# Performance work log

Hardware: AMD Instinct MI355X
Metric: run time of the kernel (lower is better)

## Reference

```python
import jax, jax.numpy as jnp
import numpy as np

B, C, W, H = 16, 256, 32, 32  # L = W*H = 1024
NUM_HEAD = 4
DIM_HEAD = C  # dim_head defaults to in_channels


def setup_inputs() -> dict:
    key = jax.random.key(0)
    ks = jax.random.split(key, 6)
    s = 0.02  # small init scale, like trained linear weights
    return {
        "x": jax.random.normal(ks[0], (B, C, W, H), dtype=jnp.float32),
        "Wq": jax.random.normal(ks[1], (NUM_HEAD, DIM_HEAD, C), dtype=jnp.float32) * s,
        "Wk": jax.random.normal(ks[2], (NUM_HEAD, DIM_HEAD, C), dtype=jnp.float32) * s,
        "Wv": jax.random.normal(ks[3], (NUM_HEAD, DIM_HEAD, C), dtype=jnp.float32) * s,
        "Wo_w": jax.random.normal(ks[4], (C, NUM_HEAD * DIM_HEAD), dtype=jnp.float32) * s,
        "Wo_b": jax.random.normal(ks[5], (C,), dtype=jnp.float32) * s,
    }


def reference(x, Wq, Wk, Wv, Wo_w, Wo_b):
    b, c, w, h = x.shape
    L = w * h
    # [b,c,w,h] -> [b,L,c]
    xs = jnp.transpose(x, (0, 2, 3, 1)).reshape(b, L, c)
    # per-head projections (torch Linear: y = x @ W^T), batched over heads
    Q = jnp.einsum('blc,hdc->bhld', xs, Wq)
    K = jnp.einsum('blc,hdc->bhld', xs, Wk)
    V = jnp.einsum('blc,hdc->bhld', xs, Wv)
    # no softmax: scores = Q K^T, heads = scores V
    scores = jnp.einsum('bhld,bhmd->bhlm', Q, K)  # [b,H,L,L]
    heads = jnp.einsum('bhlm,bhmd->bhld', scores, V)  # [b,H,L,d]
    # concat heads along channel dim -> [b,L,H*d], then output projection
    cat = jnp.transpose(heads, (0, 2, 1, 3)).reshape(b, L, -1)
    z = cat @ Wo_w.T + Wo_b  # [b,L,c]
    return jnp.transpose(z, (0, 2, 1)).reshape(b, c, w, h)
```

## Files before the change

### kernel.cpp

```cpp
#include <hip/hip_runtime.h>
#include <hip/hip_bf16.h>

typedef __attribute__((ext_vector_type(8))) short s8v;
typedef __attribute__((ext_vector_type(4))) float f4v;

__device__ __forceinline__ ushort f2bf(float f) {
    __hip_bfloat16 h = __float2bfloat16(f);
    return __builtin_bit_cast(ushort, h);
}

__device__ __forceinline__ int fsw(int row) { return ((row >> 1) ^ (row >> 3)) & 3; }

__device__ __forceinline__ void gload16(const ushort* g, ushort* l) {
    __builtin_amdgcn_global_load_lds(
        (const __attribute__((address_space(1))) unsigned*)g,
        (__attribute__((address_space(3))) unsigned*)l, 16, 0, 0);
}

__device__ __forceinline__ void cvtw16(ushort* p, float4 a, float4 b) {
    s8v u;
    u[0] = (short)f2bf(a.x); u[1] = (short)f2bf(a.y);
    u[2] = (short)f2bf(a.z); u[3] = (short)f2bf(a.w);
    u[4] = (short)f2bf(b.x); u[5] = (short)f2bf(b.y);
    u[6] = (short)f2bf(b.z); u[7] = (short)f2bf(b.w);
    *(s8v*)p = u;
}

__device__ __forceinline__ void scatw(ushort* L, int c8, int d, float4 a, float4 b) {
    float v[8] = { a.x, a.y, a.z, a.w, b.x, b.y, b.z, b.w };
#pragma unroll
    for (int i = 0; i < 8; ++i) {
        int row = c8 + i;
        L[row * 32 + (((d >> 3) ^ fsw(row)) << 3) + (d & 7)] = f2bf(v[i]);
    }
}

__device__ __forceinline__ void gemmS(
    const float* __restrict__ Xb, ushort* lds, int row0, int col0,
    ushort* __restrict__ S, int mirror) {
    const int NT = 16;
    const int tid = threadIdx.x, wave = tid >> 6, lane = tid & 63;
    const int g = wave >> 2, w4 = wave & 3;
    const int wr = w4 >> 1, wc = w4 & 1;
    const int rA = lane & 15, kg = lane >> 4;
    const int tg = tid & 255;
    const int srow = tg >> 2, slot = tg & 3;
    const int kb = g * (NT * 32);
    ushort* LA = lds + g * 16384;
    ushort* LB = LA + 8192;
    const int wadr = srow * 32 + ((slot ^ fsw(srow)) << 3);
    const float* gx = Xb + (size_t)(row0 + srow) * 1024 + kb + slot * 8;
    const float* gy = Xb + (size_t)(col0 + srow) * 1024 + kb + slot * 8;
    f4v acc[2][2] = {};
    __syncthreads();

    float4 bx[4][2], by[4][2];
#pragma unroll
    for (int p = 0; p < 3; ++p) {
        bx[p][0] = *(const float4*)(gx + p * 32);
        bx[p][1] = *(const float4*)(gx + p * 32 + 4);
        by[p][0] = *(const float4*)(gy + p * 32);
        by[p][1] = *(const float4*)(gy + p * 32 + 4);
    }
    cvtw16(LA + wadr, bx[0][0], bx[0][1]);
    cvtw16(LB + wadr, by[0][0], by[0][1]);

#pragma unroll
    for (int t = 0; t < NT; ++t) {
        if (t + 3 < NT) {
            const int bi = (t + 3) & 3;
            bx[bi][0] = *(const float4*)(gx + (t + 3) * 32);
            bx[bi][1] = *(const float4*)(gx + (t + 3) * 32 + 4);
            by[bi][0] = *(const float4*)(gy + (t + 3) * 32);
            by[bi][1] = *(const float4*)(gy + (t + 3) * 32 + 4);
        }
        if (t + 1 < NT) {
            const int bi = (t + 1) & 3;
            cvtw16(LA + ((t + 1) & 3) * 2048 + wadr, bx[bi][0], bx[bi][1]);
            cvtw16(LB + ((t + 1) & 3) * 2048 + wadr, by[bi][0], by[bi][1]);
        }
        asm volatile("s_waitcnt lgkmcnt(0)" ::: "memory");
        __builtin_amdgcn_s_barrier();
        __builtin_amdgcn_sched_barrier(0);
        const ushort* pa = LA + (t & 3) * 2048;
        const ushort* pb = LB + (t & 3) * 2048;
        s8v a[2], b[2];
#pragma unroll
        for (int m = 0; m < 2; ++m) {
            int row = wr * 32 + m * 16 + rA;
            a[m] = *(const s8v*)&pa[row * 32 + ((kg ^ fsw(row)) << 3)];
        }
#pragma unroll
        for (int n = 0; n < 2; ++n) {
            int row = wc * 32 + n * 16 + rA;
            b[n] = *(const s8v*)&pb[row * 32 + ((kg ^ fsw(row)) << 3)];
        }
#pragma unroll
        for (int m = 0; m < 2; ++m)
#pragma unroll
            for (int n = 0; n < 2; ++n)
                acc[m][n] = __builtin_amdgcn_mfma_f32_16x16x32_bf16(a[m], b[n], acc[m][n], 0, 0, 0);
    }
    __syncthreads();
    float* red = (float*)lds;
    if (g == 1) {
#pragma unroll
        for (int m = 0; m < 2; ++m)
#pragma unroll
            for (int n = 0; n < 2; ++n)
                *(f4v*)&red[(w4 * 64 + lane) * 16 + (m * 2 + n) * 4] = acc[m][n];
    }
    __syncthreads();
    if (g == 0) {
        int r4 = (lane >> 4) * 4, cl = lane & 15;
#pragma unroll
        for (int m = 0; m < 2; ++m)
#pragma unroll
            for (int n = 0; n < 2; ++n) {
                f4v o = *(const f4v*)&red[(w4 * 64 + lane) * 16 + (m * 2 + n) * 4];
                f4v s = acc[m][n] + o;
                int row = row0 + wr * 32 + m * 16 + r4;
                int col = col0 + wc * 32 + n * 16 + cl;
                ushort4 tv = { f2bf(s[0]), f2bf(s[1]), f2bf(s[2]), f2bf(s[3]) };
                S[(size_t)(row + 0) * 256 + col] = tv.x;
                S[(size_t)(row + 1) * 256 + col] = tv.y;
                S[(size_t)(row + 2) * 256 + col] = tv.z;
                S[(size_t)(row + 3) * 256 + col] = tv.w;
                if (mirror)
                    *(ushort4*)&S[(size_t)col * 256 + row] = tv;
            }
    }
}

template<int XT>
__device__ __forceinline__ void gemmWT(
    const float* __restrict__ Xw, const float* __restrict__ Yw,
    ushort* lds, int row0, int col0, ushort* __restrict__ O, int ldo) {
    const int NT = 4;
    const int tid = threadIdx.x, wave = tid >> 6, lane = tid & 63;
    const int g = wave >> 2, w4 = wave & 3;
    const int wr = w4 >> 1, wc = w4 & 1;
    const int rA = lane & 15, kg = lane >> 4;
    const int tg = tid & 255;
    const int kb = g * 128;
    ushort* LA = lds + g * 16384;
    ushort* LB = LA + 8192;
    const int dT = tg >> 3, c8 = (tg & 7) * 8;
    const int srow = tg >> 2, slot = tg & 3;
    const int wadr = srow * 32 + ((slot ^ fsw(srow)) << 3);
    f4v acc[2][2] = {};
    __syncthreads();

    float4 bx[4][2], by[4][2];
#pragma unroll
    for (int p = 0; p < 3; ++p) {
        if (XT) {
            bx[p][0] = *(const float4*)(Xw + (size_t)(kb + p * 32 + dT) * 256 + row0 + c8);
            bx[p][1] = *(const float4*)(Xw + (size_t)(kb + p * 32 + dT) * 256 + row0 + c8 + 4);
        } else {
            bx[p][0] = *(const float4*)(Xw + (size_t)(row0 + srow) * 1024 + kb + p * 32 + slot * 8);
            bx[p][1] = *(const float4*)(Xw + (size_t)(row0 + srow) * 1024 + kb + p * 32 + slot * 8 + 4);
        }
        by[p][0] = *(const float4*)(Yw + (size_t)(kb + p * 32 + dT) * 256 + col0 + c8);
        by[p][1] = *(const float4*)(Yw + (size_t)(kb + p * 32 + dT) * 256 + col0 + c8 + 4);
    }
    if (XT) scatw(LA, c8, dT, bx[0][0], bx[0][1]);
    else    cvtw16(LA + wadr, bx[0][0], bx[0][1]);
    scatw(LB, c8, dT, by[0][0], by[0][1]);

#pragma unroll
    for (int t = 0; t < NT; ++t) {
        if (t + 3 < NT) {
            const int bi = (t + 3) & 3;
            if (XT) {
                bx[bi][0] = *(const float4*)(Xw + (size_t)(kb + (t + 3) * 32 + dT) * 256 + row0 + c8);
                bx[bi][1] = *(const float4*)(Xw + (size_t)(kb + (t + 3) * 32 + dT) * 256 + row0 + c8 + 4);
            } else {
                bx[bi][0] = *(const float4*)(Xw + (size_t)(row0 + srow) * 1024 + kb + (t + 3) * 32 + slot * 8);
                bx[bi][1] = *(const float4*)(Xw + (size_t)(row0 + srow) * 1024 + kb + (t + 3) * 32 + slot * 8 + 4);
            }
            by[bi][0] = *(const float4*)(Yw + (size_t)(kb + (t + 3) * 32 + dT) * 256 + col0 + c8);
            by[bi][1] = *(const float4*)(Yw + (size_t)(kb + (t + 3) * 32 + dT) * 256 + col0 + c8 + 4);
        }
        if (t + 1 < NT) {
            const int bi = (t + 1) & 3;
            ushort* la = LA + ((t + 1) & 3) * 2048;
            ushort* lb = LB + ((t + 1) & 3) * 2048;
            if (XT) scatw(la, c8, dT, bx[bi][0], bx[bi][1]);
            else    cvtw16(la + wadr, bx[bi][0], bx[bi][1]);
            scatw(lb, c8, dT, by[bi][0], by[bi][1]);
        }
        asm volatile("s_waitcnt lgkmcnt(0)" ::: "memory");
        __builtin_amdgcn_s_barrier();
        __builtin_amdgcn_sched_barrier(0);
        const ushort* pa = LA + (t & 3) * 2048;
        const ushort* pb = LB + (t & 3) * 2048;
        s8v a[2], b[2];
#pragma unroll
        for (int m = 0; m < 2; ++m) {
            int row = wr * 32 + m * 16 + rA;
            a[m] = *(const s8v*)&pa[row * 32 + ((kg ^ fsw(row)) << 3)];
        }
#pragma unroll
        for (int n = 0; n < 2; ++n) {
            int row = wc * 32 + n * 16 + rA;
            b[n] = *(const s8v*)&pb[row * 32 + ((kg ^ fsw(row)) << 3)];
        }
#pragma unroll
        for (int m = 0; m < 2; ++m)
#pragma unroll
            for (int n = 0; n < 2; ++n)
                acc[m][n] = __builtin_amdgcn_mfma_f32_16x16x32_bf16(a[m], b[n], acc[m][n], 0, 0, 0);
    }
    __syncthreads();
    float* red = (float*)lds;
    if (g == 1) {
#pragma unroll
        for (int m = 0; m < 2; ++m)
#pragma unroll
            for (int n = 0; n < 2; ++n)
                *(f4v*)&red[(w4 * 64 + lane) * 16 + (m * 2 + n) * 4] = acc[m][n];
    }
    __syncthreads();
    if (g == 0) {
        int r4 = (lane >> 4) * 4, cl = lane & 15;
#pragma unroll
        for (int m = 0; m < 2; ++m)
#pragma unroll
            for (int n = 0; n < 2; ++n) {
                f4v o = *(const f4v*)&red[(w4 * 64 + lane) * 16 + (m * 2 + n) * 4];
                f4v s = acc[m][n] + o;
                int row = row0 + wr * 32 + m * 16 + r4;
                int col = col0 + wc * 32 + n * 16 + cl;
#pragma unroll
                for (int r = 0; r < 4; ++r)
                    O[(size_t)(row + r) * ldo + col] = f2bf(s[r]);
            }
    }
}

__device__ __forceinline__ void gemm64x8(
    const ushort* __restrict__ Xb, const ushort* __restrict__ Yb,
    int ldx, int ldy, ushort* lds, int row0, int col0, int K,
    ushort* __restrict__ O, int ldo) {
    const int tid = threadIdx.x, wave = tid >> 6, lane = tid & 63;
    const int g = wave >> 2, w4 = wave & 3;
    const int wr = w4 >> 1, wc = w4 & 1;
    const int rA = lane & 15, kg = lane >> 4;
    const int srow = w4 * 16 + (lane >> 2);
    const int scol = ((lane & 3) ^ fsw(srow)) * 8;
    const int K2 = K >> 1, NT = K2 >> 5, kb = g * K2;
    ushort* LA = lds + g * 16384;
    ushort* LB = LA + 8192;
    f4v acc[2][2] = {};
    __syncthreads();
    const ushort* gx = Xb + (size_t)(row0 + srow) * ldx + kb + scol;
    const ushort* gy = Yb + (size_t)(col0 + srow) * ldy + kb + scol;
    gload16(gx,      LA + w4 * 512);
    gload16(gy,      LB + w4 * 512);
    gload16(gx + 32, LA + 2048 + w4 * 512);
    gload16(gy + 32, LB + 2048 + w4 * 512);
    for (int t = 0; t < NT; ++t) {
        if (t + 2 < NT) {
            int s2 = (t + 2) & 3, kt = (t + 2) << 5;
            gload16(gx + kt, LA + s2 * 2048 + w4 * 512);
            gload16(gy + kt, LB + s2 * 2048 + w4 * 512);
            asm volatile("s_waitcnt vmcnt(4)" ::: "memory");
        } else if (t + 1 < NT) {
            asm volatile("s_waitcnt vmcnt(2)" ::: "memory");
        } else {
            asm volatile("s_waitcnt vmcnt(0)" ::: "memory");
        }
        __builtin_amdgcn_s_barrier();
        __builtin_amdgcn_sched_barrier(0);
        const ushort* pa = LA + (t & 3) * 2048;
        const ushort* pb = LB + (t & 3) * 2048;
        s8v a[2], b[2];
#pragma unroll
        for (int m = 0; m < 2; ++m) {
            int row = wr * 32 + m * 16 + rA;
            a[m] = *(const s8v*)&pa[row * 32 + ((kg ^ fsw(row)) << 3)];
        }
#pragma unroll
        for (int n = 0; n < 2; ++n) {
            int row = wc * 32 + n * 16 + rA;
            b[n] = *(const s8v*)&pb[row * 32 + ((kg ^ fsw(row)) << 3)];
        }
#pragma unroll
        for (int m = 0; m < 2; ++m)
#pragma unroll
            for (int n = 0; n < 2; ++n)
                acc[m][n] = __builtin_amdgcn_mfma_f32_16x16x32_bf16(a[m], b[n], acc[m][n], 0, 0, 0);
    }
    __syncthreads();
    float* red = (float*)lds;
    if (g == 1) {
#pragma unroll
        for (int m = 0; m < 2; ++m)
#pragma unroll
            for (int n = 0; n < 2; ++n)
                *(f4v*)&red[(w4 * 64 + lane) * 16 + (m * 2 + n) * 4] = acc[m][n];
    }
    __syncthreads();
    if (g == 0) {
        int r4 = (lane >> 4) * 4, cl = lane & 15;
#pragma unroll
        for (int m = 0; m < 2; ++m)
#pragma unroll
            for (int n = 0; n < 2; ++n) {
                f4v o = *(const f4v*)&red[(w4 * 64 + lane) * 16 + (m * 2 + n) * 4];
                f4v s = acc[m][n] + o;
                int row = row0 + wr * 32 + m * 16 + r4;
                int col = col0 + wc * 32 + n * 16 + cl;
#pragma unroll
                for (int r = 0; r < 4; ++r)
                    O[(size_t)(row + r) * ldo + col] = f2bf(s[r]);
            }
    }
}

template<int OBF>
__device__ __forceinline__ void gemm128x8(
    const ushort* __restrict__ Xb, const ushort* __restrict__ Yb,
    int ldx, int ldy, ushort* lds, int row0, int col0, int K,
    void* __restrict__ Oraw, int ldo, const float* __restrict__ bias) {
    const int tid = threadIdx.x, wave = tid >> 6, lane = tid & 63;
    const int wr = wave >> 2, wc = wave & 3;
    const int rA = lane & 15, kg = lane >> 4;
    const int srow = wave * 16 + (lane >> 2);
    const int scol = ((lane & 3) ^ fsw(srow)) * 8;
    const int NT = K >> 5;
    ushort* LA = lds;
    ushort* LB = lds + 16384;
    f4v acc[4][2] = {};
    __syncthreads();
    const ushort* gx = Xb + (size_t)(row0 + srow) * ldx + scol;
    const ushort* gy = Yb + (size_t)(col0 + srow) * ldy + scol;
#pragma unroll
    for (int p = 0; p < 2; ++p) {
        gload16(gx + p * 32, LA + p * 4096 + wave * 512);
        gload16(gy + p * 32, LB + p * 4096 + wave * 512);
    }
    for (int t = 0; t < NT; ++t) {
        if (t + 2 < NT) {
            int s2 = (t + 2) & 3, kt = (t + 2) << 5;
            gload16(gx + kt, LA + s2 * 4096 + wave * 512);
            gload16(gy + kt, LB + s2 * 4096 + wave * 512);
            asm volatile("s_waitcnt vmcnt(4)" ::: "memory");
        } else if (t + 1 < NT) {
            asm volatile("s_waitcnt vmcnt(2)" ::: "memory");
        } else {
            asm volatile("s_waitcnt vmcnt(0)" ::: "memory");
        }
        __builtin_amdgcn_s_barrier();
        __builtin_amdgcn_sched_barrier(0);
        const ushort* pa = LA + (t & 3) * 4096;
        const ushort* pb = LB + (t & 3) * 4096;
        s8v a[4], b[2];
#pragma unroll
        for (int m = 0; m < 4; ++m) {
            int row = wr * 64 + m * 16 + rA;
            a[m] = *(const s8v*)&pa[row * 32 + ((kg ^ fsw(row)) << 3)];
        }
#pragma unroll
        for (int n = 0; n < 2; ++n) {
            int row = wc * 32 + n * 16 + rA;
            b[n] = *(const s8v*)&pb[row * 32 + ((kg ^ fsw(row)) << 3)];
        }
#pragma unroll
        for (int m = 0; m < 4; ++m)
#pragma unroll
            for (int n = 0; n < 2; ++n)
                acc[m][n] = __builtin_amdgcn_mfma_f32_16x16x32_bf16(a[m], b[n], acc[m][n], 0, 0, 0);
    }
    int r4 = (lane >> 4) * 4, cl = lane & 15;
    if (OBF) {
        ushort* O = (ushort*)Oraw;
#pragma unroll
        for (int m = 0; m < 4; ++m)
#pragma unroll
            for (int n = 0; n < 2; ++n) {
                int row = row0 + wr * 64 + m * 16 + r4;
                int col = col0 + wc * 32 + n * 16 + cl;
#pragma unroll
                for (int r = 0; r < 4; ++r)
                    O[(size_t)(row + r) * ldo + col] = f2bf(acc[m][n][r]);
            }
    } else {
        float* O = (float*)Oraw;
#pragma unroll
        for (int m = 0; m < 4; ++m)
#pragma unroll
            for (int n = 0; n < 2; ++n) {
                int row = row0 + wr * 64 + m * 16 + r4;
                int col = col0 + wc * 32 + n * 16 + cl;
#pragma unroll
                for (int r = 0; r < 4; ++r)
                    O[(size_t)(row + r) * ldo + col] = acc[m][n][r] + bias[row + r];
            }
    }
}

__global__ __launch_bounds__(512, 2) void kSP(
    const float* __restrict__ x, const float* __restrict__ Wq,
    const float* __restrict__ Wk,
    ushort* __restrict__ S16, ushort* __restrict__ A16, ushort* __restrict__ xlc) {
    __shared__ __align__(16) ushort lds[32768];
    const int bid = blockIdx.x, tid = threadIdx.x;
    if (bid < 160) {
        int xcd = bid & 7, idx = bid >> 3;
        int b = 2 * xcd + (idx >= 10);
        int tri = (idx >= 10) ? idx - 10 : idx;
        int ti, tj;
        if (tri < 4)      { ti = 0; tj = tri; }
        else if (tri < 7) { ti = 1; tj = tri - 3; }
        else if (tri < 9) { ti = 2; tj = tri - 5; }
        else              { ti = 3; tj = 3; }
        const float* xb = x + (size_t)b * 262144;
        gemmS(xb, lds, ti * 64, tj * 64, S16 + (size_t)b * 65536, ti != tj);
    } else if (bid < 224) {
        int q = bid - 160, h = q >> 4, t2 = q & 15;
        gemmWT<1>(Wq + (size_t)h * 65536, Wk + (size_t)h * 65536, lds,
                  (t2 >> 2) * 64, (t2 & 3) * 64, A16 + (size_t)h * 65536, 256);
    } else {
        ushort (*t)[72] = (ushort(*)[72])lds;
        int r = tid >> 3, c0 = (tid & 7) * 8;
#pragma unroll
        for (int rr = 0; rr < 4; ++rr) {
            int jid = (bid - 224) + 256 * rr;
            __syncthreads();
            int lt = jid & 15, ct = (jid >> 4) & 3, b2 = jid >> 6;
            size_t so = (size_t)(b2 * 256 + ct * 64 + r) * 1024 + lt * 64 + c0;
            float4 v0 = *(const float4*)(x + so);
            float4 v1 = *(const float4*)(x + so + 4);
            ushort4 u0 = { f2bf(v0.x), f2bf(v0.y), f2bf(v0.z), f2bf(v0.w) };
            ushort4 u1 = { f2bf(v1.x), f2bf(v1.y), f2bf(v1.z), f2bf(v1.w) };
            *(ushort4*)&t[r][c0] = u0;
            *(ushort4*)&t[r][c0 + 4] = u1;
            __syncthreads();
            size_t dof = (size_t)(b2 * 1024 + lt * 64 + r) * 256 + ct * 64 + c0;
            ushort4 w0 = { t[c0][r], t[c0 + 1][r], t[c0 + 2][r], t[c0 + 3][r] };
            ushort4 w1 = { t[c0 + 4][r], t[c0 + 5][r], t[c0 + 6][r], t[c0 + 7][r] };
            *(ushort4*)(xlc + dof) = w0;
            *(ushort4*)(xlc + dof + 4) = w1;
        }
    }
}

__global__ __launch_bounds__(512, 2) void kT1(
    const ushort* __restrict__ A16, const ushort* __restrict__ S16,
    const float* __restrict__ Wo, const float* __restrict__ Wv,
    ushort* __restrict__ T1, ushort* __restrict__ BT) {
    __shared__ __align__(16) ushort lds[32768];
    int j = blockIdx.x;
    if (j < 256) {
        int xcd = j & 7, idx = j >> 3;
        int b = 2 * xcd + (idx >> 4), h = (idx >> 2) & 3, tile = idx & 3;
        gemm128x8<1>(A16 + (size_t)h * 65536, S16 + (size_t)b * 65536, 256, 256, lds,
                     (tile >> 1) * 128, (tile & 1) * 128, 256,
                     T1 + (size_t)b * 262144 + h * 256, 1024, nullptr);
    } else {
        int q = j - 256, h = q >> 4, t2 = q & 15;
        gemmWT<0>(Wo + (size_t)h * 256, Wv + (size_t)h * 65536, lds,
                  (t2 >> 2) * 64, (t2 & 3) * 64, BT + (size_t)h * 256, 1024);
    }
}

__global__ __launch_bounds__(512, 2) void kGT(
    const ushort* __restrict__ BT, const ushort* __restrict__ T1,
    ushort* __restrict__ GT) {
    __shared__ __align__(16) ushort lds[32768];
    int j = blockIdx.x, xcd = j & 7, idx = j >> 3;
    int b = 2 * xcd + (idx >> 4), tile = idx & 15;
    gemm64x8(BT, T1 + (size_t)b * 262144, 1024, 1024, lds,
             (tile >> 2) * 64, (tile & 3) * 64, 1024, GT + (size_t)b * 65536, 256);
}

__global__ __launch_bounds__(512, 2) void kOUT(
    const ushort* __restrict__ GT, const ushort* __restrict__ xlc,
    float* __restrict__ out, const float* __restrict__ bias) {
    __shared__ __align__(16) ushort lds[32768];
    int j = blockIdx.x, xcd = j & 7, idx = j >> 3;
    int b = 2 * xcd + (idx >> 4), tile = idx & 15;
    gemm128x8<0>(GT + (size_t)b * 65536, xlc + (size_t)b * 262144, 256, 256, lds,
                 (tile >> 3) * 128, (tile & 7) * 128, 256,
                 out + (size_t)b * 262144, 1024, bias);
}

extern "C" void kernel_launch(void* const* d_in, const int* in_sizes, int n_in,
                              void* d_out, int out_size, void* d_ws, size_t ws_size,
                              hipStream_t stream) {
    const float* x  = (const float*)d_in[0];
    const float* Wq = (const float*)d_in[1];
    const float* Wk = (const float*)d_in[2];
    const float* Wv = (const float*)d_in[3];
    const float* Wo = (const float*)d_in[4];
    const float* Wb = (const float*)d_in[5];

    char* ws = (char*)d_ws;
    ushort* T1  = (ushort*)(ws + 0);
    ushort* xlc = (ushort*)(ws + 8388608);
    ushort* S16 = (ushort*)(ws + 16777216);
    ushort* GT  = (ushort*)(ws + 20971520);
    ushort* A16 = (ushort*)(ws + 25165824);
    ushort* BT  = (ushort*)(ws + 26214400);

    hipLaunchKernelGGL(kSP,  dim3(480), dim3(512), 0, stream, x, Wq, Wk, S16, A16, xlc);
    hipLaunchKernelGGL(kT1,  dim3(320), dim3(512), 0, stream, A16, S16, Wo, Wv, T1, BT);
    hipLaunchKernelGGL(kGT,  dim3(256), dim3(512), 0, stream, BT, T1, GT);
    hipLaunchKernelGGL(kOUT, dim3(256), dim3(512), 0, stream, GT, xlc, (float*)d_out, Wb);
}
```

Baseline: 39.82 us.

## Replace LDS-staged GEMMs with direct-to-register per-wave MFMA tiles; move BT build into kSP

Three bf16 GEMM kernels (kT1, kGT, kOUT) stop staging tiles through LDS with global_load_lds, barriers and a split-K reduction. Each wave now computes its own 64x64 or 32x32 output tile, loading MFMA operand fragments straight from global memory into a register ring buffer a few k-steps ahead. Blocks shrink to 256 threads. The Wo·Wv (BT) GEMM moves from kT1 into the first kernel kSP, so it runs alongside the other weight preprocessing. The trade is no LDS operand reuse across waves, more global/L2 traffic with uncoalesced 16-byte row loads, and more register pressure.

```diff
diff --git a/kernel.cpp b/kernel.cpp
--- a/kernel.cpp
+++ b/kernel.cpp
@@ -10,12 +10,6 @@
 }
 
 __device__ __forceinline__ int fsw(int row) { return ((row >> 1) ^ (row >> 3)) & 3; }
-
-__device__ __forceinline__ void gload16(const ushort* g, ushort* l) {
-    __builtin_amdgcn_global_load_lds(
-        (const __attribute__((address_space(1))) unsigned*)g,
-        (__attribute__((address_space(3))) unsigned*)l, 16, 0, 0);
-}
 
 __device__ __forceinline__ void cvtw16(ushort* p, float4 a, float4 b) {
     s8v u;
@@ -34,6 +28,8 @@
         L[row * 32 + (((d >> 3) ^ fsw(row)) << 3) + (d & 7)] = f2bf(v[i]);
     }
 }
+
+__device__ __forceinline__ s8v ld8(const ushort* p) { return *(const s8v*)p; }
 
 __device__ __forceinline__ void gemmS(
     const float* __restrict__ Xb, ushort* lds, int row0, int col0,
@@ -239,149 +235,49 @@
     }
 }
 
-__device__ __forceinline__ void gemm64x8(
-    const ushort* __restrict__ Xb, const ushort* __restrict__ Yb,
-    int ldx, int ldy, ushort* lds, int row0, int col0, int K,
-    ushort* __restrict__ O, int ldo) {
-    const int tid = threadIdx.x, wave = tid >> 6, lane = tid & 63;
-    const int g = wave >> 2, w4 = wave & 3;
-    const int wr = w4 >> 1, wc = w4 & 1;
+template<int NT, int OBF>
+__device__ __forceinline__ void gemmDF64(
+    const ushort* __restrict__ X, const ushort* __restrict__ Y,
+    int ldx, int ldy, int row0, int col0,
+    void* __restrict__ Oraw, int ldo, const float* __restrict__ bias) {
+    const int lane = threadIdx.x & 63;
     const int rA = lane & 15, kg = lane >> 4;
-    const int srow = w4 * 16 + (lane >> 2);
-    const int scol = ((lane & 3) ^ fsw(srow)) * 8;
-    const int K2 = K >> 1, NT = K2 >> 5, kb = g * K2;
-    ushort* LA = lds + g * 16384;
-    ushort* LB = LA + 8192;
-    f4v acc[2][2] = {};
-    __syncthreads();
-    const ushort* gx = Xb + (size_t)(row0 + srow) * ldx + kb + scol;
-    const ushort* gy = Yb + (size_t)(col0 + srow) * ldy + kb + scol;
-    gload16(gx,      LA + w4 * 512);
-    gload16(gy,      LB + w4 * 512);
-    gload16(gx + 32, LA + 2048 + w4 * 512);
-    gload16(gy + 32, LB + 2048 + w4 * 512);
+    const ushort* ax = X + (size_t)(row0 + rA) * ldx + kg * 8;
+    const ushort* by = Y + (size_t)(col0 + rA) * ldy + kg * 8;
+    f4v acc[4][4] = {};
+    s8v a[3][4], b[3][4];
+#pragma unroll
+    for (int p = 0; p < 2; ++p) {
+#pragma unroll
+        for (int m = 0; m < 4; ++m) a[p][m] = ld8(ax + (size_t)m * 16 * ldx + p * 32);
+#pragma unroll
+        for (int n = 0; n < 4; ++n) b[p][n] = ld8(by + (size_t)n * 16 * ldy + p * 32);
+    }
+#pragma unroll
     for (int t = 0; t < NT; ++t) {
         if (t + 2 < NT) {
-            int s2 = (t + 2) & 3, kt = (t + 2) << 5;
-            gload16(gx + kt, LA + s2 * 2048 + w4 * 512);
-            gload16(gy + kt, LB + s2 * 2048 + w4 * 512);
-            asm volatile("s_waitcnt vmcnt(4)" ::: "memory");
-        } else if (t + 1 < NT) {
-            asm volatile("s_waitcnt vmcnt(2)" ::: "memory");
-        } else {
-            asm volatile("s_waitcnt vmcnt(0)" ::: "memory");
-        }
-        __builtin_amdgcn_s_barrier();
-        __builtin_amdgcn_sched_barrier(0);
-        const ushort* pa = LA + (t & 3) * 2048;
-        const ushort* pb = LB + (t & 3) * 2048;
-        s8v a[2], b[2];
-#pragma unroll
-        for (int m = 0; m < 2; ++m) {
-            int row = wr * 32 + m * 16 + rA;
-            a[m] = *(const s8v*)&pa[row * 32 + ((kg ^ fsw(row)) << 3)];
-        }
-#pragma unroll
-        for (int n = 0; n < 2; ++n) {
-            int row = wc * 32 + n * 16 + rA;
-            b[n] = *(const s8v*)&pb[row * 32 + ((kg ^ fsw(row)) << 3)];
-        }
-#pragma unroll
-        for (int m = 0; m < 2; ++m)
-#pragma unroll
-            for (int n = 0; n < 2; ++n)
-                acc[m][n] = __builtin_amdgcn_mfma_f32_16x16x32_bf16(a[m], b[n], acc[m][n], 0, 0, 0);
-    }
-    __syncthreads();
-    float* red = (float*)lds;
-    if (g == 1) {
-#pragma unroll
-        for (int m = 0; m < 2; ++m)
-#pragma unroll
-            for (int n = 0; n < 2; ++n)
-                *(f4v*)&red[(w4 * 64 + lane) * 16 + (m * 2 + n) * 4] = acc[m][n];
-    }
-    __syncthreads();
-    if (g == 0) {
-        int r4 = (lane >> 4) * 4, cl = lane & 15;
-#pragma unroll
-        for (int m = 0; m < 2; ++m)
-#pragma unroll
-            for (int n = 0; n < 2; ++n) {
-                f4v o = *(const f4v*)&red[(w4 * 64 + lane) * 16 + (m * 2 + n) * 4];
-                f4v s = acc[m][n] + o;
-                int row = row0 + wr * 32 + m * 16 + r4;
-                int col = col0 + wc * 32 + n * 16 + cl;
-#pragma unroll
-                for (int r = 0; r < 4; ++r)
-                    O[(size_t)(row + r) * ldo + col] = f2bf(s[r]);
-            }
-    }
-}
-
-template<int OBF>
-__device__ __forceinline__ void gemm128x8(
-    const ushort* __restrict__ Xb, const ushort* __restrict__ Yb,
-    int ldx, int ldy, ushort* lds, int row0, int col0, int K,
-    void* __restrict__ Oraw, int ldo, const float* __restrict__ bias) {
-    const int tid = threadIdx.x, wave = tid >> 6, lane = tid & 63;
-    const int wr = wave >> 2, wc = wave & 3;
-    const int rA = lane & 15, kg = lane >> 4;
-    const int srow = wave * 16 + (lane >> 2);
-    const int scol = ((lane & 3) ^ fsw(srow)) * 8;
-    const int NT = K >> 5;
-    ushort* LA = lds;
-    ushort* LB = lds + 16384;
-    f4v acc[4][2] = {};
-    __syncthreads();
-    const ushort* gx = Xb + (size_t)(row0 + srow) * ldx + scol;
-    const ushort* gy = Yb + (size_t)(col0 + srow) * ldy + scol;
-#pragma unroll
-    for (int p = 0; p < 2; ++p) {
-        gload16(gx + p * 32, LA + p * 4096 + wave * 512);
-        gload16(gy + p * 32, LB + p * 4096 + wave * 512);
-    }
-    for (int t = 0; t < NT; ++t) {
-        if (t + 2 < NT) {
-            int s2 = (t + 2) & 3, kt = (t + 2) << 5;
-            gload16(gx + kt, LA + s2 * 4096 + wave * 512);
-            gload16(gy + kt, LB + s2 * 4096 + wave * 512);
-            asm volatile("s_waitcnt vmcnt(4)" ::: "memory");
-        } else if (t + 1 < NT) {
-            asm volatile("s_waitcnt vmcnt(2)" ::: "memory");
-        } else {
-            asm volatile("s_waitcnt vmcnt(0)" ::: "memory");
-        }
-        __builtin_amdgcn_s_barrier();
-        __builtin_amdgcn_sched_barrier(0);
-        const ushort* pa = LA + (t & 3) * 4096;
-        const ushort* pb = LB + (t & 3) * 4096;
-        s8v a[4], b[2];
-#pragma unroll
-        for (int m = 0; m < 4; ++m) {
-            int row = wr * 64 + m * 16 + rA;
-            a[m] = *(const s8v*)&pa[row * 32 + ((kg ^ fsw(row)) << 3)];
-        }
-#pragma unroll
-        for (int n = 0; n < 2; ++n) {
-            int row = wc * 32 + n * 16 + rA;
-            b[n] = *(const s8v*)&pb[row * 32 + ((kg ^ fsw(row)) << 3)];
-        }
+            const int s = (t + 2) % 3;
+#pragma unroll
+            for (int m = 0; m < 4; ++m) a[s][m] = ld8(ax + (size_t)m * 16 * ldx + (t + 2) * 32);
+#pragma unroll
+            for (int n = 0; n < 4; ++n) b[s][n] = ld8(by + (size_t)n * 16 * ldy + (t + 2) * 32);
+        }
+        const int c = t % 3;
 #pragma unroll
         for (int m = 0; m < 4; ++m)
 #pragma unroll
-            for (int n = 0; n < 2; ++n)
-                acc[m][n] = __builtin_amdgcn_mfma_f32_16x16x32_bf16(a[m], b[n], acc[m][n], 0, 0, 0);
-    }
-    int r4 = (lane >> 4) * 4, cl = lane & 15;
+            for (int n = 0; n < 4; ++n)
+                acc[m][n] = __builtin_amdgcn_mfma_f32_16x16x32_bf16(a[c][m], b[c][n], acc[m][n], 0, 0, 0);
+    }
+    const int r4 = (lane >> 4) * 4, cl = lane & 15;
     if (OBF) {
         ushort* O = (ushort*)Oraw;
 #pragma unroll
         for (int m = 0; m < 4; ++m)
 #pragma unroll
-            for (int n = 0; n < 2; ++n) {
-                int row = row0 + wr * 64 + m * 16 + r4;
-                int col = col0 + wc * 32 + n * 16 + cl;
+            for (int n = 0; n < 4; ++n) {
+                int row = row0 + m * 16 + r4;
+                int col = col0 + n * 16 + cl;
 #pragma unroll
                 for (int r = 0; r < 4; ++r)
                     O[(size_t)(row + r) * ldo + col] = f2bf(acc[m][n][r]);
@@ -391,9 +287,9 @@
 #pragma unroll
         for (int m = 0; m < 4; ++m)
 #pragma unroll
-            for (int n = 0; n < 2; ++n) {
-                int row = row0 + wr * 64 + m * 16 + r4;
-                int col = col0 + wc * 32 + n * 16 + cl;
+            for (int n = 0; n < 4; ++n) {
+                int row = row0 + m * 16 + r4;
+                int col = col0 + n * 16 + cl;
 #pragma unroll
                 for (int r = 0; r < 4; ++r)
                     O[(size_t)(row + r) * ldo + col] = acc[m][n][r] + bias[row + r];
@@ -401,10 +297,58 @@
     }
 }
 
+template<int NT>
+__device__ __forceinline__ void gemmDF32(
+    const ushort* __restrict__ X, const ushort* __restrict__ Y,
+    int ldx, int ldy, int row0, int col0, ushort* __restrict__ O, int ldo) {
+    const int lane = threadIdx.x & 63;
+    const int rA = lane & 15, kg = lane >> 4;
+    const ushort* ax = X + (size_t)(row0 + rA) * ldx + kg * 8;
+    const ushort* by = Y + (size_t)(col0 + rA) * ldy + kg * 8;
+    f4v acc[2][2] = {};
+    s8v a[4][2], b[4][2];
+#pragma unroll
+    for (int p = 0; p < 3; ++p) {
+#pragma unroll
+        for (int m = 0; m < 2; ++m) a[p][m] = ld8(ax + (size_t)m * 16 * ldx + p * 32);
+#pragma unroll
+        for (int n = 0; n < 2; ++n) b[p][n] = ld8(by + (size_t)n * 16 * ldy + p * 32);
+    }
+#pragma unroll
+    for (int t = 0; t < NT; ++t) {
+        if (t + 3 < NT) {
+            const int s = (t + 3) & 3;
+#pragma unroll
+            for (int m = 0; m < 2; ++m) a[s][m] = ld8(ax + (size_t)m * 16 * ldx + (t + 3) * 32);
+#pragma unroll
+            for (int n = 0; n < 2; ++n) b[s][n] = ld8(by + (size_t)n * 16 * ldy + (t + 3) * 32);
+        }
+        const int c = t & 3;
+#pragma unroll
+        for (int m = 0; m < 2; ++m)
+#pragma unroll
+            for (int n = 0; n < 2; ++n)
+                acc[m][n] = __builtin_amdgcn_mfma_f32_16x16x32_bf16(a[c][m], b[c][n], acc[m][n], 0, 0, 0);
+    }
+    const int r4 = (lane >> 4) * 4, cl = lane & 15;
+#pragma unroll
+    for (int m = 0; m < 2; ++m)
+#pragma unroll
+        for (int n = 0; n < 2; ++n) {
+            int row = row0 + m * 16 + r4;
+            int col = col0 + n * 16 + cl;
+#pragma unroll
+            for (int r = 0; r < 4; ++r)
+                O[(size_t)(row + r) * ldo + col] = f2bf(acc[m][n][r]);
+        }
+}
+
 __global__ __launch_bounds__(512, 2) void kSP(
     const float* __restrict__ x, const float* __restrict__ Wq,
-    const float* __restrict__ Wk,
-    ushort* __restrict__ S16, ushort* __restrict__ A16, ushort* __restrict__ xlc) {
+    const float* __restrict__ Wk, const float* __restrict__ Wv,
+    const float* __restrict__ Wo,
+    ushort* __restrict__ S16, ushort* __restrict__ A16,
+    ushort* __restrict__ BT, ushort* __restrict__ xlc) {
     __shared__ __align__(16) ushort lds[32768];
     const int bid = blockIdx.x, tid = threadIdx.x;
     if (bid < 160) {
@@ -422,12 +366,16 @@
         int q = bid - 160, h = q >> 4, t2 = q & 15;
         gemmWT<1>(Wq + (size_t)h * 65536, Wk + (size_t)h * 65536, lds,
                   (t2 >> 2) * 64, (t2 & 3) * 64, A16 + (size_t)h * 65536, 256);
+    } else if (bid < 288) {
+        int q = bid - 224, h = q >> 4, t2 = q & 15;
+        gemmWT<0>(Wo + (size_t)h * 256, Wv + (size_t)h * 65536, lds,
+                  (t2 >> 2) * 64, (t2 & 3) * 64, BT + (size_t)h * 256, 1024);
     } else {
         ushort (*t)[72] = (ushort(*)[72])lds;
         int r = tid >> 3, c0 = (tid & 7) * 8;
 #pragma unroll
         for (int rr = 0; rr < 4; ++rr) {
-            int jid = (bid - 224) + 256 * rr;
+            int jid = (bid - 288) + 256 * rr;
             __syncthreads();
             int lt = jid & 15, ct = (jid >> 4) & 3, b2 = jid >> 6;
             size_t so = (size_t)(b2 * 256 + ct * 64 + r) * 1024 + lt * 64 + c0;
@@ -447,44 +395,40 @@
     }
 }
 
-__global__ __launch_bounds__(512, 2) void kT1(
+__global__ __launch_bounds__(256, 2) void kT1(
     const ushort* __restrict__ A16, const ushort* __restrict__ S16,
-    const float* __restrict__ Wo, const float* __restrict__ Wv,
-    ushort* __restrict__ T1, ushort* __restrict__ BT) {
-    __shared__ __align__(16) ushort lds[32768];
-    int j = blockIdx.x;
-    if (j < 256) {
-        int xcd = j & 7, idx = j >> 3;
-        int b = 2 * xcd + (idx >> 4), h = (idx >> 2) & 3, tile = idx & 3;
-        gemm128x8<1>(A16 + (size_t)h * 65536, S16 + (size_t)b * 65536, 256, 256, lds,
-                     (tile >> 1) * 128, (tile & 1) * 128, 256,
-                     T1 + (size_t)b * 262144 + h * 256, 1024, nullptr);
-    } else {
-        int q = j - 256, h = q >> 4, t2 = q & 15;
-        gemmWT<0>(Wo + (size_t)h * 256, Wv + (size_t)h * 65536, lds,
-                  (t2 >> 2) * 64, (t2 & 3) * 64, BT + (size_t)h * 256, 1024);
-    }
-}
-
-__global__ __launch_bounds__(512, 2) void kGT(
+    ushort* __restrict__ T1) {
+    int bid = blockIdx.x, wave = threadIdx.x >> 6;
+    int xcd = bid & 7, idx = bid >> 3;
+    int b = 2 * xcd + (idx >> 4);
+    int tile = (idx & 15) * 4 + wave;
+    int h = tile >> 4, r = (tile >> 2) & 3, c = tile & 3;
+    gemmDF64<8, 1>(A16 + (size_t)h * 65536, S16 + (size_t)b * 65536, 256, 256,
+                   r * 64, c * 64, T1 + (size_t)b * 262144 + h * 256, 1024, nullptr);
+}
+
+__global__ __launch_bounds__(256, 2) void kGT(
     const ushort* __restrict__ BT, const ushort* __restrict__ T1,
     ushort* __restrict__ GT) {
-    __shared__ __align__(16) ushort lds[32768];
-    int j = blockIdx.x, xcd = j & 7, idx = j >> 3;
-    int b = 2 * xcd + (idx >> 4), tile = idx & 15;
-    gemm64x8(BT, T1 + (size_t)b * 262144, 1024, 1024, lds,
-             (tile >> 2) * 64, (tile & 3) * 64, 1024, GT + (size_t)b * 65536, 256);
-}
-
-__global__ __launch_bounds__(512, 2) void kOUT(
+    int bid = blockIdx.x, wave = threadIdx.x >> 6;
+    int xcd = bid & 7, idx = bid >> 3;
+    int b = 2 * xcd + (idx >> 4);
+    int tile = (idx & 15) * 4 + wave;
+    int rt = tile >> 3, ct = tile & 7;
+    gemmDF32<32>(BT, T1 + (size_t)b * 262144, 1024, 1024,
+                 rt * 32, ct * 32, GT + (size_t)b * 65536, 256);
+}
+
+__global__ __launch_bounds__(256, 2) void kOUT(
     const ushort* __restrict__ GT, const ushort* __restrict__ xlc,
     float* __restrict__ out, const float* __restrict__ bias) {
-    __shared__ __align__(16) ushort lds[32768];
-    int j = blockIdx.x, xcd = j & 7, idx = j >> 3;
-    int b = 2 * xcd + (idx >> 4), tile = idx & 15;
-    gemm128x8<0>(GT + (size_t)b * 65536, xlc + (size_t)b * 262144, 256, 256, lds,
-                 (tile >> 3) * 128, (tile & 7) * 128, 256,
-                 out + (size_t)b * 262144, 1024, bias);
+    int bid = blockIdx.x, wave = threadIdx.x >> 6;
+    int xcd = bid & 7, idx = bid >> 3;
+    int b = 2 * xcd + (idx >> 4);
+    int tile = (idx & 15) * 4 + wave;
+    int rt = tile >> 4, ct = tile & 15;
+    gemmDF64<8, 0>(GT + (size_t)b * 65536, xlc + (size_t)b * 262144, 256, 256,
+                   rt * 64, ct * 64, out + (size_t)b * 262144, 1024, bias);
 }
 
 extern "C" void kernel_launch(void* const* d_in, const int* in_sizes, int n_in,
@@ -505,8 +449,9 @@
     ushort* A16 = (ushort*)(ws + 25165824);
     ushort* BT  = (ushort*)(ws + 26214400);
 
-    hipLaunchKernelGGL(kSP,  dim3(480), dim3(512), 0, stream, x, Wq, Wk, S16, A16, xlc);
-    hipLaunchKernelGGL(kT1,  dim3(320), dim3(512), 0, stream, A16, S16, Wo, Wv, T1, BT);
-    hipLaunchKernelGGL(kGT,  dim3(256), dim3(512), 0, stream, BT, T1, GT);
-    hipLaunchKernelGGL(kOUT, dim3(256), dim3(512), 0, stream, GT, xlc, (float*)d_out, Wb);
-}
+    hipLaunchKernelGGL(kSP,  dim3(544), dim3(512), 0, stream,
+                       x, Wq, Wk, Wv, Wo, S16, A16, BT, xlc);
+    hipLaunchKernelGGL(kT1,  dim3(256), dim3(256), 0, stream, A16, S16, T1);
+    hipLaunchKernelGGL(kGT,  dim3(256), dim3(256), 0, stream, BT, T1, GT);
+    hipLaunchKernelGGL(kOUT, dim3(256), dim3(256), 0, stream, GT, xlc, (float*)d_out, Wb);
+}
```

Result: slower. 61.67 us (+54.9%).

## Shrink T1/OUT GEMM tiles to 64x64 and move BT weight fold into first kernel

Applied to the files above, without the earlier changes.

Replaces the 128x128, 8-wave GEMM tile used by kT1 and kOUT with a 64x64 tile on 4 waves, with a compile-time K loop that is fully unrolled. This quadruples the block count, to 1024 per launch, for better CU fill. The Wo·Wv fold (BT) moves from kT1 into kSP as extra blocks so kT1 is a uniform GEMM launch. Smaller tiles give less operand reuse per loaded byte and more redundant global/L2 traffic.

```diff
diff --git a/kernel.cpp b/kernel.cpp
--- a/kernel.cpp
+++ b/kernel.cpp
@@ -319,33 +319,31 @@
     }
 }
 
-template<int OBF>
-__device__ __forceinline__ void gemm128x8(
-    const ushort* __restrict__ Xb, const ushort* __restrict__ Yb,
-    int ldx, int ldy, ushort* lds, int row0, int col0, int K,
+template<int NT, int OBF>
+__device__ __forceinline__ void gemm64q(
+    const ushort* __restrict__ X, const ushort* __restrict__ Y,
+    int ldx, int ldy, ushort* lds, int row0, int col0,
     void* __restrict__ Oraw, int ldo, const float* __restrict__ bias) {
     const int tid = threadIdx.x, wave = tid >> 6, lane = tid & 63;
-    const int wr = wave >> 2, wc = wave & 3;
+    const int wr = wave >> 1, wc = wave & 1;
     const int rA = lane & 15, kg = lane >> 4;
     const int srow = wave * 16 + (lane >> 2);
     const int scol = ((lane & 3) ^ fsw(srow)) * 8;
-    const int NT = K >> 5;
     ushort* LA = lds;
-    ushort* LB = lds + 16384;
-    f4v acc[4][2] = {};
-    __syncthreads();
-    const ushort* gx = Xb + (size_t)(row0 + srow) * ldx + scol;
-    const ushort* gy = Yb + (size_t)(col0 + srow) * ldy + scol;
-#pragma unroll
-    for (int p = 0; p < 2; ++p) {
-        gload16(gx + p * 32, LA + p * 4096 + wave * 512);
-        gload16(gy + p * 32, LB + p * 4096 + wave * 512);
-    }
+    ushort* LB = lds + 8192;
+    f4v acc[2][2] = {};
+    const ushort* gx = X + (size_t)(row0 + srow) * ldx + scol;
+    const ushort* gy = Y + (size_t)(col0 + srow) * ldy + scol;
+    gload16(gx,      LA + wave * 512);
+    gload16(gy,      LB + wave * 512);
+    gload16(gx + 32, LA + 2048 + wave * 512);
+    gload16(gy + 32, LB + 2048 + wave * 512);
+#pragma unroll
     for (int t = 0; t < NT; ++t) {
         if (t + 2 < NT) {
             int s2 = (t + 2) & 3, kt = (t + 2) << 5;
-            gload16(gx + kt, LA + s2 * 4096 + wave * 512);
-            gload16(gy + kt, LB + s2 * 4096 + wave * 512);
+            gload16(gx + kt, LA + s2 * 2048 + wave * 512);
+            gload16(gy + kt, LB + s2 * 2048 + wave * 512);
             asm volatile("s_waitcnt vmcnt(4)" ::: "memory");
         } else if (t + 1 < NT) {
             asm volatile("s_waitcnt vmcnt(2)" ::: "memory");
@@ -354,12 +352,12 @@
         }
         __builtin_amdgcn_s_barrier();
         __builtin_amdgcn_sched_barrier(0);
-        const ushort* pa = LA + (t & 3) * 4096;
-        const ushort* pb = LB + (t & 3) * 4096;
-        s8v a[4], b[2];
-#pragma unroll
-        for (int m = 0; m < 4; ++m) {
-            int row = wr * 64 + m * 16 + rA;
+        const ushort* pa = LA + (t & 3) * 2048;
+        const ushort* pb = LB + (t & 3) * 2048;
+        s8v a[2], b[2];
+#pragma unroll
+        for (int m = 0; m < 2; ++m) {
+            int row = wr * 32 + m * 16 + rA;
             a[m] = *(const s8v*)&pa[row * 32 + ((kg ^ fsw(row)) << 3)];
         }
 #pragma unroll
@@ -368,19 +366,19 @@
             b[n] = *(const s8v*)&pb[row * 32 + ((kg ^ fsw(row)) << 3)];
         }
 #pragma unroll
-        for (int m = 0; m < 4; ++m)
+        for (int m = 0; m < 2; ++m)
 #pragma unroll
             for (int n = 0; n < 2; ++n)
                 acc[m][n] = __builtin_amdgcn_mfma_f32_16x16x32_bf16(a[m], b[n], acc[m][n], 0, 0, 0);
     }
-    int r4 = (lane >> 4) * 4, cl = lane & 15;
+    const int r4 = (lane >> 4) * 4, cl = lane & 15;
     if (OBF) {
         ushort* O = (ushort*)Oraw;
 #pragma unroll
-        for (int m = 0; m < 4; ++m)
+        for (int m = 0; m < 2; ++m)
 #pragma unroll
             for (int n = 0; n < 2; ++n) {
-                int row = row0 + wr * 64 + m * 16 + r4;
+                int row = row0 + wr * 32 + m * 16 + r4;
                 int col = col0 + wc * 32 + n * 16 + cl;
 #pragma unroll
                 for (int r = 0; r < 4; ++r)
@@ -389,10 +387,10 @@
     } else {
         float* O = (float*)Oraw;
 #pragma unroll
-        for (int m = 0; m < 4; ++m)
+        for (int m = 0; m < 2; ++m)
 #pragma unroll
             for (int n = 0; n < 2; ++n) {
-                int row = row0 + wr * 64 + m * 16 + r4;
+                int row = row0 + wr * 32 + m * 16 + r4;
                 int col = col0 + wc * 32 + n * 16 + cl;
 #pragma unroll
                 for (int r = 0; r < 4; ++r)
@@ -403,8 +401,10 @@
 
 __global__ __launch_bounds__(512, 2) void kSP(
     const float* __restrict__ x, const float* __restrict__ Wq,
-    const float* __restrict__ Wk,
-    ushort* __restrict__ S16, ushort* __restrict__ A16, ushort* __restrict__ xlc) {
+    const float* __restrict__ Wk, const float* __restrict__ Wv,
+    const float* __restrict__ Wo,
+    ushort* __restrict__ S16, ushort* __restrict__ A16,
+    ushort* __restrict__ BT, ushort* __restrict__ xlc) {
     __shared__ __align__(16) ushort lds[32768];
     const int bid = blockIdx.x, tid = threadIdx.x;
     if (bid < 160) {
@@ -422,12 +422,16 @@
         int q = bid - 160, h = q >> 4, t2 = q & 15;
         gemmWT<1>(Wq + (size_t)h * 65536, Wk + (size_t)h * 65536, lds,
                   (t2 >> 2) * 64, (t2 & 3) * 64, A16 + (size_t)h * 65536, 256);
+    } else if (bid < 288) {
+        int q = bid - 224, h = q >> 4, t2 = q & 15;
+        gemmWT<0>(Wo + (size_t)h * 256, Wv + (size_t)h * 65536, lds,
+                  (t2 >> 2) * 64, (t2 & 3) * 64, BT + (size_t)h * 256, 1024);
     } else {
         ushort (*t)[72] = (ushort(*)[72])lds;
         int r = tid >> 3, c0 = (tid & 7) * 8;
 #pragma unroll
         for (int rr = 0; rr < 4; ++rr) {
-            int jid = (bid - 224) + 256 * rr;
+            int jid = (bid - 288) + 256 * rr;
             __syncthreads();
             int lt = jid & 15, ct = (jid >> 4) & 3, b2 = jid >> 6;
             size_t so = (size_t)(b2 * 256 + ct * 64 + r) * 1024 + lt * 64 + c0;
@@ -447,23 +451,16 @@
     }
 }
 
-__global__ __launch_bounds__(512, 2) void kT1(
+__global__ __launch_bounds__(256, 2) void kT1(
     const ushort* __restrict__ A16, const ushort* __restrict__ S16,
-    const float* __restrict__ Wo, const float* __restrict__ Wv,
-    ushort* __restrict__ T1, ushort* __restrict__ BT) {
-    __shared__ __align__(16) ushort lds[32768];
-    int j = blockIdx.x;
-    if (j < 256) {
-        int xcd = j & 7, idx = j >> 3;
-        int b = 2 * xcd + (idx >> 4), h = (idx >> 2) & 3, tile = idx & 3;
-        gemm128x8<1>(A16 + (size_t)h * 65536, S16 + (size_t)b * 65536, 256, 256, lds,
-                     (tile >> 1) * 128, (tile & 1) * 128, 256,
-                     T1 + (size_t)b * 262144 + h * 256, 1024, nullptr);
-    } else {
-        int q = j - 256, h = q >> 4, t2 = q & 15;
-        gemmWT<0>(Wo + (size_t)h * 256, Wv + (size_t)h * 65536, lds,
-                  (t2 >> 2) * 64, (t2 & 3) * 64, BT + (size_t)h * 256, 1024);
-    }
+    ushort* __restrict__ T1) {
+    __shared__ __align__(16) ushort lds[16384];
+    int bid = blockIdx.x, xcd = bid & 7, idx = bid >> 3;
+    int b = 2 * xcd + (idx >> 6);
+    int q = idx & 63;
+    int h = q >> 4, r = (q >> 2) & 3, c = q & 3;
+    gemm64q<8, 1>(A16 + (size_t)h * 65536, S16 + (size_t)b * 65536, 256, 256, lds,
+                  r * 64, c * 64, T1 + (size_t)b * 262144 + h * 256, 1024, nullptr);
 }
 
 __global__ __launch_bounds__(512, 2) void kGT(
@@ -476,15 +473,15 @@
              (tile >> 2) * 64, (tile & 3) * 64, 1024, GT + (size_t)b * 65536, 256);
 }
 
-__global__ __launch_bounds__(512, 2) void kOUT(
+__global__ __launch_bounds__(256, 2) void kOUT(
     const ushort* __restrict__ GT, const ushort* __restrict__ xlc,
     float* __restrict__ out, const float* __restrict__ bias) {
-    __shared__ __align__(16) ushort lds[32768];
-    int j = blockIdx.x, xcd = j & 7, idx = j >> 3;
-    int b = 2 * xcd + (idx >> 4), tile = idx & 15;
-    gemm128x8<0>(GT + (size_t)b * 65536, xlc + (size_t)b * 262144, 256, 256, lds,
-                 (tile >> 3) * 128, (tile & 7) * 128, 256,
-                 out + (size_t)b * 262144, 1024, bias);
+    __shared__ __align__(16) ushort lds[16384];
+    int bid = blockIdx.x, xcd = bid & 7, idx = bid >> 3;
+    int b = 2 * xcd + (idx >> 6);
+    int q = idx & 63;
+    gemm64q<8, 0>(GT + (size_t)b * 65536, xlc + (size_t)b * 262144, 256, 256, lds,
+                  (q >> 4) * 64, (q & 15) * 64, out + (size_t)b * 262144, 1024, bias);
 }
 
 extern "C" void kernel_launch(void* const* d_in, const int* in_sizes, int n_in,
@@ -505,8 +502,9 @@
     ushort* A16 = (ushort*)(ws + 25165824);
     ushort* BT  = (ushort*)(ws + 26214400);
 
-    hipLaunchKernelGGL(kSP,  dim3(480), dim3(512), 0, stream, x, Wq, Wk, S16, A16, xlc);
-    hipLaunchKernelGGL(kT1,  dim3(320), dim3(512), 0, stream, A16, S16, Wo, Wv, T1, BT);
+    hipLaunchKernelGGL(kSP,  dim3(544), dim3(512), 0, stream,
+                       x, Wq, Wk, Wv, Wo, S16, A16, BT, xlc);
+    hipLaunchKernelGGL(kT1,  dim3(1024), dim3(256), 0, stream, A16, S16, T1);
     hipLaunchKernelGGL(kGT,  dim3(256), dim3(512), 0, stream, BT, T1, GT);
-    hipLaunchKernelGGL(kOUT, dim3(256), dim3(512), 0, stream, GT, xlc, (float*)d_out, Wb);
-}
+    hipLaunchKernelGGL(kOUT, dim3(1024), dim3(256), 0, stream, GT, xlc, (float*)d_out, Wb);
+}
```

New measurement: 39.26 us. About the same (-1.4%).
